# Performance work log

Hardware: AMD Instinct MI355X
Metric: run time of the kernel (lower is better)

## Reference

```python
import jax, jax.numpy as jnp
import numpy as np

B, S, D = 2, 2048, 4096
NH, NKV, HD = 32, 8, 128
N_REP = NH // NKV
MAX_B, MAX_S = 2, 2048


def _rope(x, cos, sin):
    # x: [b, s, h, hd]; cos/sin: [s, hd//2]
    xr = x.reshape(*x.shape[:-1], HD // 2, 2)
    xe, xo = xr[..., 0], xr[..., 1]
    c = cos[None, :, None, :]
    s = sin[None, :, None, :]
    oe = xe * c - xo * s
    oo = xe * s + xo * c
    return jnp.stack([oe, oo], axis=-1).reshape(x.shape)


def setup_inputs() -> dict:
    key = jax.random.key(0)
    ks = jax.random.split(key, 8)
    x = jax.random.normal(ks[0], (B, S, D), dtype=jnp.float32)
    # xavier-normal-ish weights (module uses identity init_method, i.e. uninitialized;
    # we use scaled gaussians for a well-conditioned reference)
    wq = jax.random.normal(ks[1], (NH * HD, D), dtype=jnp.float32) * (1.0 / np.sqrt(D))
    wk = jax.random.normal(ks[2], (NKV * HD, D), dtype=jnp.float32) * (1.0 / np.sqrt(D))
    wv = jax.random.normal(ks[3], (NKV * HD, D), dtype=jnp.float32) * (1.0 / np.sqrt(D))
    wo = jax.random.normal(ks[4], (D, NH * HD), dtype=jnp.float32) * (1.0 / np.sqrt(D))
    # rotary freqs (llama-style, theta=500000)
    theta = 500000.0
    inv = 1.0 / (theta ** (np.arange(0, HD, 2, dtype=np.float32) / HD))  # [hd/2]
    t = np.arange(S, dtype=np.float32)
    ang = np.outer(t, inv)  # [S, hd/2]
    freqs_cos = jnp.asarray(np.cos(ang), dtype=jnp.float32)
    freqs_sin = jnp.asarray(np.sin(ang), dtype=jnp.float32)
    # causal mask
    mask = jnp.where(jnp.tril(jnp.ones((S, S), dtype=bool)), 0.0, -jnp.inf).astype(jnp.float32)
    cache_k = jnp.zeros((MAX_B, MAX_S, NKV, HD), dtype=jnp.float32)
    cache_v = jnp.zeros((MAX_B, MAX_S, NKV, HD), dtype=jnp.float32)
    return {"x": x, "wq": wq, "wk": wk, "wv": wv, "wo": wo,
            "freqs_cos": freqs_cos, "freqs_sin": freqs_sin,
            "mask": mask, "cache_k": cache_k, "cache_v": cache_v,
            "start_pos": 0}


def reference(x, wq, wk, wv, wo, freqs_cos, freqs_sin, mask, cache_k, cache_v, start_pos):
    bsz, seqlen, _ = x.shape
    xq = jnp.einsum('bsd,qd->bsq', x, wq).reshape(bsz, seqlen, NH, HD)
    xk = jnp.einsum('bsd,kd->bsk', x, wk).reshape(bsz, seqlen, NKV, HD)
    xv = jnp.einsum('bsd,vd->bsv', x, wv).reshape(bsz, seqlen, NKV, HD)
    xq = _rope(xq, freqs_cos, freqs_sin)
    xk = _rope(xk, freqs_cos, freqs_sin)
    # KV-cache update then read back valid prefix
    cache_k = jax.lax.dynamic_update_slice(cache_k, xk, (0, start_pos, 0, 0))
    cache_v = jax.lax.dynamic_update_slice(cache_v, xv, (0, start_pos, 0, 0))
    kvlen = start_pos + seqlen
    keys = cache_k[:bsz, :kvlen]    # [b, T, nkv, hd]
    values = cache_v[:bsz, :kvlen]
    # GQA repeat_kv
    keys = jnp.broadcast_to(keys[:, :, :, None, :], (bsz, kvlen, NKV, N_REP, HD)).reshape(bsz, kvlen, NH, HD)
    values = jnp.broadcast_to(values[:, :, :, None, :], (bsz, kvlen, NKV, N_REP, HD)).reshape(bsz, kvlen, NH, HD)
    scores = jnp.einsum('bqhd,bkhd->bhqk', xq, keys) / np.sqrt(HD)
    scores = scores + mask[None, None, :, :]
    probs = jax.nn.softmax(scores, axis=-1)
    out = jnp.einsum('bhqk,bkhd->bqhd', probs, values).reshape(bsz, seqlen, NH * HD)
    return jnp.einsum('bsq,dq->bsd', out, wo)
```

## Files before the change

### kernel.cpp

```cpp
#include <hip/hip_runtime.h>
#include <hip/hip_bf16.h>

#define B_ 2
#define S_ 2048
#define D_ 4096
#define NH_ 32
#define NKV_ 8
#define HD_ 128
#define M_ (B_ * S_)

typedef __bf16 bf16x8_t __attribute__((ext_vector_type(8)));
typedef float f32x4_t __attribute__((ext_vector_type(4)));

__device__ __forceinline__ void gload16(const __bf16* g, __bf16* l) {
  __builtin_amdgcn_global_load_lds(
      (const __attribute__((address_space(1))) void*)g,
      (__attribute__((address_space(3))) void*)l, 16, 0, 0);
}

__global__ __launch_bounds__(256) void convert_main(const float* __restrict__ x,
                                                    const float* __restrict__ wq,
                                                    const float* __restrict__ wk,
                                                    const float* __restrict__ wv,
                                                    __bf16* __restrict__ xb,
                                                    __bf16* __restrict__ wqkv) {
  size_t c = (size_t)blockIdx.x * 256 + threadIdx.x;
  const float* src;
  __bf16* dst;
  if (c < 2097152) { src = x + c * 8; dst = xb + c * 8; }
  else if (c < 4194304) { c -= 2097152; src = wq + c * 8; dst = wqkv + c * 8; }
  else if (c < 4718592) { c -= 4194304; src = wk + c * 8; dst = wqkv + 16777216 + c * 8; }
  else { c -= 4718592; src = wv + c * 8; dst = wqkv + 20971520 + c * 8; }
  const float4* s4 = reinterpret_cast<const float4*>(src);
  float4 a = s4[0], b = s4[1];
  bf16x8_t t;
  t[0] = (__bf16)a.x; t[1] = (__bf16)a.y; t[2] = (__bf16)a.z; t[3] = (__bf16)a.w;
  t[4] = (__bf16)b.x; t[5] = (__bf16)b.y; t[6] = (__bf16)b.z; t[7] = (__bf16)b.w;
  *reinterpret_cast<bf16x8_t*>(dst) = t;
}

__global__ __launch_bounds__(256) void convert_wo(const float* __restrict__ wo,
                                                  __bf16* __restrict__ wob) {
  size_t c = (size_t)blockIdx.x * 256 + threadIdx.x;
  const float4* s4 = reinterpret_cast<const float4*>(wo + c * 8);
  float4 a = s4[0], b = s4[1];
  bf16x8_t t;
  t[0] = (__bf16)a.x; t[1] = (__bf16)a.y; t[2] = (__bf16)a.z; t[3] = (__bf16)a.w;
  t[4] = (__bf16)b.x; t[5] = (__bf16)b.y; t[6] = (__bf16)b.z; t[7] = (__bf16)b.w;
  *reinterpret_cast<bf16x8_t*>(wob + c * 8) = t;
}

template <bool SPLIT, bool OUTF32>
__global__ __launch_bounds__(256) void gemm_bt(const __bf16* __restrict__ A,
                                               const __bf16* __restrict__ Bm,
                                               void* __restrict__ C0,
                                               void* __restrict__ C1,
                                               int N, int K) {
  __shared__ __attribute__((aligned(16))) __bf16 As[128 * 32];
  __shared__ __attribute__((aligned(16))) __bf16 Bs[128 * 32];
  const int tid = threadIdx.x;
  const int lane = tid & 63;
  const int w = tid >> 6;
  const int lo = lane & 15;
  const int hi = lane >> 4;
  const int wm = (w & 1) * 64;
  const int wn = (w >> 1) * 64;
  const int m0 = blockIdx.y * 128;
  const int n0 = blockIdx.x * 128;

  const int srow = w * 32 + (lane >> 2);
  const int scol = (lane & 3) * 8;
  const __bf16* ga0 = A + (size_t)(m0 + srow) * K + scol;
  const __bf16* ga1 = A + (size_t)(m0 + srow + 16) * K + scol;
  const __bf16* gb0 = Bm + (size_t)(n0 + srow) * K + scol;
  const __bf16* gb1 = Bm + (size_t)(n0 + srow + 16) * K + scol;
  __bf16* la0 = &As[(w * 32) * 32];
  __bf16* la1 = &As[(w * 32 + 16) * 32];
  __bf16* lb0 = &Bs[(w * 32) * 32];
  __bf16* lb1 = &Bs[(w * 32 + 16) * 32];

  f32x4_t acc[4][4] = {};

  for (int k0 = 0; k0 < K; k0 += 32) {
    __syncthreads();
    gload16(ga0 + k0, la0);
    gload16(ga1 + k0, la1);
    gload16(gb0 + k0, lb0);
    gload16(gb1 + k0, lb1);
    __syncthreads();
    bf16x8_t af[4], bfr[4];
#pragma unroll
    for (int mi = 0; mi < 4; mi++)
      af[mi] = *reinterpret_cast<const bf16x8_t*>(&As[(wm + mi * 16 + lo) * 32 + hi * 8]);
#pragma unroll
    for (int ni = 0; ni < 4; ni++)
      bfr[ni] = *reinterpret_cast<const bf16x8_t*>(&Bs[(wn + ni * 16 + lo) * 32 + hi * 8]);
#pragma unroll
    for (int mi = 0; mi < 4; mi++)
#pragma unroll
      for (int ni = 0; ni < 4; ni++)
        acc[mi][ni] = __builtin_amdgcn_mfma_f32_16x16x32_bf16(af[mi], bfr[ni], acc[mi][ni], 0, 0, 0);
  }

  __bf16* Cb = nullptr;
  float* Cf = nullptr;
  int ldc, nb;
  if constexpr (SPLIT) {
    if (n0 < 4096) { Cb = (__bf16*)C0; ldc = 4096; nb = n0; }
    else { Cb = (__bf16*)C1; ldc = 2048; nb = n0 - 4096; }
  } else {
    ldc = N; nb = n0;
    if constexpr (OUTF32) Cf = (float*)C0; else Cb = (__bf16*)C0;
  }
#pragma unroll
  for (int mi = 0; mi < 4; mi++) {
    const int mrow = m0 + wm + mi * 16 + hi * 4;
#pragma unroll
    for (int ni = 0; ni < 4; ni++) {
      const int ncol = nb + wn + ni * 16 + lo;
#pragma unroll
      for (int r = 0; r < 4; r++) {
        if constexpr (OUTF32)
          Cf[(size_t)(mrow + r) * ldc + ncol] = acc[mi][ni][r];
        else
          Cb[(size_t)(mrow + r) * ldc + ncol] = (__bf16)acc[mi][ni][r];
      }
    }
  }
}

typedef __bf16 bf16x2_t __attribute__((ext_vector_type(2)));
__global__ __launch_bounds__(256) void rope_kernel(__bf16* __restrict__ q,
                                                   __bf16* __restrict__ kv,
                                                   const float* __restrict__ fcos,
                                                   const float* __restrict__ fsin) {
  const int p = blockIdx.x * 256 + threadIdx.x;
  const int j = p & 63;
  int rem = p >> 6;
  const int hh = rem % (NH_ + NKV_);
  rem /= (NH_ + NKV_);
  const int s = rem % S_;
  const int b = rem / S_;
  const float c = fcos[s * 64 + j];
  const float sn = fsin[s * 64 + j];
  __bf16* base;
  if (hh < NH_)
    base = q + ((size_t)(b * S_ + s) * NH_ + hh) * HD_ + 2 * j;
  else
    base = kv + (size_t)(b * S_ + s) * 2048 + (hh - NH_) * HD_ + 2 * j;
  bf16x2_t xv = *reinterpret_cast<const bf16x2_t*>(base);
  const float xe = (float)xv[0], xo = (float)xv[1];
  bf16x2_t ov;
  ov[0] = (__bf16)(xe * c - xo * sn);
  ov[1] = (__bf16)(xe * sn + xo * c);
  *reinterpret_cast<bf16x2_t*>(base) = ov;
}

__global__ __launch_bounds__(256) void attn_kernel(const __bf16* __restrict__ q,
                                                   const __bf16* __restrict__ kv,
                                                   __bf16* __restrict__ o) {
  const int flat = blockIdx.x + (blockIdx.y << 3) + (blockIdx.z << 8);
  const int hkv = flat & 7;
  const int idx = flat >> 3;
  const int h = hkv * 4 + ((idx >> 3) & 3);
  const int b = idx >> 5;
  const int xpair = idx & 7;

  const int tid = threadIdx.x;
  const int lane = tid & 63;
  const int w = tid >> 6;
  const int lo = lane & 15;
  const int hi = lane >> 4;

  __shared__ __attribute__((aligned(16))) __bf16 Ks[64 * 132];
  __shared__ __attribute__((aligned(16))) __bf16 Vt[128 * 68];
  __shared__ __attribute__((aligned(16))) __bf16 Ps[4][32 * 68];

  bf16x8_t ones;
#pragma unroll
  for (int e = 0; e < 8; e++) ones[e] = (__bf16)1.0f;

  constexpr float SC = 0.08838834764831845f * 1.44269504088896f;

  const __bf16* kvb = kv + (size_t)b * S_ * 2048 + hkv * 128;
  int kkey[4], khc[4], vkey[4], vhc[4];
#pragma unroll
  for (int i = 0; i < 4; i++) {
    const int c = tid + i * 256;
    kkey[i] = c >> 4; khc[i] = c & 15;
    vkey[i] = c & 63; vhc[i] = c >> 6;
  }

  bf16x8_t kreg[4], vreg[4];

  for (int pass = 0; pass < 2; pass++) {
    const int qt = pass ? (15 - xpair) : xpair;
    const int q0 = qt * 128;

    bf16x8_t qf[2][4];
#pragma unroll
    for (int mi = 0; mi < 2; mi++) {
      const size_t qbase = ((size_t)(b * S_ + q0 + w * 32 + mi * 16 + lo) * NH_ + h) * HD_;
#pragma unroll
      for (int ks = 0; ks < 4; ks++)
        qf[mi][ks] = *reinterpret_cast<const bf16x8_t*>(q + qbase + ks * 32 + hi * 8);
    }

    f32x4_t o_acc[2][8] = {};
    f32x4_t l_acc[2] = {};
    float m_prev[2][4];
#pragma unroll
    for (int mi = 0; mi < 2; mi++)
#pragma unroll
      for (int r = 0; r < 4; r++) m_prev[mi][r] = -1e30f;

    const int nkt = qt * 2 + 2;

#pragma unroll
    for (int i = 0; i < 4; i++) {
      kreg[i] = *reinterpret_cast<const bf16x8_t*>(kvb + (size_t)kkey[i] * 2048 + khc[i] * 8);
      vreg[i] = *reinterpret_cast<const bf16x8_t*>(kvb + (size_t)vkey[i] * 2048 + 1024 + vhc[i] * 8);
    }

    for (int kt = 0; kt < nkt; kt++) {
      const int kt0 = kt * 64;
      __syncthreads();
#pragma unroll
      for (int i = 0; i < 4; i++)
        *reinterpret_cast<bf16x8_t*>(&Ks[kkey[i] * 132 + khc[i] * 8]) = kreg[i];
#pragma unroll
      for (int i = 0; i < 4; i++)
#pragma unroll
        for (int e = 0; e < 8; e++) Vt[(vhc[i] * 8 + e) * 68 + vkey[i]] = vreg[i][e];
      __syncthreads();
      if (kt + 1 < nkt) {
        const int nt0 = (kt + 1) * 64;
#pragma unroll
        for (int i = 0; i < 4; i++) {
          kreg[i] = *reinterpret_cast<const bf16x8_t*>(kvb + (size_t)(nt0 + kkey[i]) * 2048 + khc[i] * 8);
          vreg[i] = *reinterpret_cast<const bf16x8_t*>(kvb + (size_t)(nt0 + vkey[i]) * 2048 + 1024 + vhc[i] * 8);
        }
      }

      f32x4_t s_acc[2][4] = {};
      __builtin_amdgcn_s_setprio(1);
#pragma unroll
      for (int ks = 0; ks < 4; ks++) {
        bf16x8_t kf[4];
#pragma unroll
        for (int t = 0; t < 4; t++)
          kf[t] = *reinterpret_cast<const bf16x8_t*>(&Ks[(t * 16 + lo) * 132 + ks * 32 + hi * 8]);
#pragma unroll
        for (int mi = 0; mi < 2; mi++)
#pragma unroll
          for (int t = 0; t < 4; t++)
            s_acc[mi][t] = __builtin_amdgcn_mfma_f32_16x16x32_bf16(qf[mi][ks], kf[t], s_acc[mi][t], 0, 0, 0);
      }
      __builtin_amdgcn_s_setprio(0);

#pragma unroll
      for (int mi = 0; mi < 2; mi++) {
        const int rowbase = q0 + w * 32 + mi * 16;
        const bool need_mask = (kt0 + 63) > rowbase;
        float sv[4][4];
#pragma unroll
        for (int t = 0; t < 4; t++)
#pragma unroll
          for (int r = 0; r < 4; r++) {
            float val = s_acc[mi][t][r] * SC;
            if (need_mask && (kt0 + t * 16 + lo) > (rowbase + hi * 4 + r)) val = -1e30f;
            sv[t][r] = val;
          }
        float alpha[4], mnew[4];
#pragma unroll
        for (int r = 0; r < 4; r++) {
          float mx = fmaxf(fmaxf(sv[0][r], sv[1][r]), fmaxf(sv[2][r], sv[3][r]));
#pragma unroll
          for (int off = 1; off < 16; off <<= 1) mx = fmaxf(mx, __shfl_xor(mx, off));
          mnew[r] = fmaxf(m_prev[mi][r], mx);
          alpha[r] = __builtin_amdgcn_exp2f(m_prev[mi][r] - mnew[r]);
          m_prev[mi][r] = mnew[r];
        }
#pragma unroll
        for (int t = 0; t < 4; t++)
#pragma unroll
          for (int r = 0; r < 4; r++)
            Ps[w][(mi * 16 + hi * 4 + r) * 68 + t * 16 + lo] =
                (__bf16)__builtin_amdgcn_exp2f(sv[t][r] - mnew[r]);
#pragma unroll
        for (int t8 = 0; t8 < 8; t8++)
#pragma unroll
          for (int r = 0; r < 4; r++) o_acc[mi][t8][r] *= alpha[r];
#pragma unroll
        for (int r = 0; r < 4; r++) l_acc[mi][r] *= alpha[r];
      }

      __builtin_amdgcn_s_setprio(1);
#pragma unroll
      for (int ks2 = 0; ks2 < 2; ks2++) {
        bf16x8_t pf[2];
#pragma unroll
        for (int mi = 0; mi < 2; mi++)
          pf[mi] = *reinterpret_cast<const bf16x8_t*>(&Ps[w][(mi * 16 + lo) * 68 + ks2 * 32 + hi * 8]);
#pragma unroll
        for (int mi = 0; mi < 2; mi++)
          l_acc[mi] = __builtin_amdgcn_mfma_f32_16x16x32_bf16(pf[mi], ones, l_acc[mi], 0, 0, 0);
#pragma unroll
        for (int t8 = 0; t8 < 8; t8++) {
          bf16x8_t vf = *reinterpret_cast<const bf16x8_t*>(&Vt[(t8 * 16 + lo) * 68 + ks2 * 32 + hi * 8]);
#pragma unroll
          for (int mi = 0; mi < 2; mi++)
            o_acc[mi][t8] = __builtin_amdgcn_mfma_f32_16x16x32_bf16(pf[mi], vf, o_acc[mi][t8], 0, 0, 0);
        }
      }
      __builtin_amdgcn_s_setprio(0);
    }

#pragma unroll
    for (int mi = 0; mi < 2; mi++)
#pragma unroll
      for (int r = 0; r < 4; r++) {
        const float inv = 1.0f / l_acc[mi][r];
        const int qr = q0 + w * 32 + mi * 16 + hi * 4 + r;
        const size_t obase = ((size_t)(b * S_ + qr) * NH_ + h) * HD_;
#pragma unroll
        for (int t8 = 0; t8 < 8; t8++)
          o[obase + t8 * 16 + lo] = (__bf16)(o_acc[mi][t8][r] * inv);
      }
  }
}

extern "C" void kernel_launch(void* const* d_in, const int* in_sizes, int n_in,
                              void* d_out, int out_size, void* d_ws, size_t ws_size,
                              hipStream_t stream) {
  const float* x = (const float*)d_in[0];
  const float* wq = (const float*)d_in[1];
  const float* wk = (const float*)d_in[2];
  const float* wv = (const float*)d_in[3];
  const float* wo = (const float*)d_in[4];
  const float* fcos = (const float*)d_in[5];
  const float* fsin = (const float*)d_in[6];
  float* out = (float*)d_out;

  __bf16* xb   = (__bf16*)d_ws;
  __bf16* wqkv = xb + (size_t)16777216;
  __bf16* qb   = (__bf16*)d_ws + (size_t)41943040;
  __bf16* kvb  = qb + (size_t)16777216;
  __bf16* wob  = xb;
  __bf16* ab   = wqkv;

  convert_main<<<20480, 256, 0, stream>>>(x, wq, wk, wv, xb, wqkv);
  gemm_bt<true, false><<<dim3(48, 32), 256, 0, stream>>>(xb, wqkv, qb, kvb, 6144, D_);
  convert_wo<<<8192, 256, 0, stream>>>(wo, wob);
  rope_kernel<<<(M_ * (NH_ + NKV_) * (HD_ / 2)) / 256, 256, 0, stream>>>(qb, kvb, fcos, fsin);
  attn_kernel<<<dim3(8, NH_, B_), 256, 0, stream>>>(qb, kvb, ab);
  gemm_bt<false, true><<<dim3(32, 32), 256, 0, stream>>>(ab, wob, out, nullptr, D_, D_);
}
```

Measured before the change: 991.3 us.

## Write V transposed from QKV GEMM and keep P in registers for PV

The QKV GEMM epilogue now writes V directly in a transposed [b, channel, seq] layout and K into its own buffer, so attention can stage V into LDS with vector stores instead of a scalar transpose. Attention computes S^T (K as the A operand), which lets the bf16 probabilities stay in registers as the B operand of 16x16x16 MFMAs, dropping the per-wave P LDS round-trip and the ones-vector MFMA used for row sums. Row max and sum now need only two cross-lane shuffles. The trade-offs are strided 8-byte global writes for V in the GEMM epilogue and twice as many smaller-K MFMAs in the PV product.

```diff
diff --git a/kernel.cpp b/kernel.cpp
--- a/kernel.cpp
+++ b/kernel.cpp
@@ -10,13 +10,29 @@
 #define M_ (B_ * S_)
 
 typedef __bf16 bf16x8_t __attribute__((ext_vector_type(8)));
+typedef __bf16 bf16x4_t __attribute__((ext_vector_type(4)));
+typedef __bf16 bf16x2_t __attribute__((ext_vector_type(2)));
 typedef float f32x4_t __attribute__((ext_vector_type(4)));
+typedef short short4_t __attribute__((ext_vector_type(4)));
 
 __device__ __forceinline__ void gload16(const __bf16* g, __bf16* l) {
   __builtin_amdgcn_global_load_lds(
       (const __attribute__((address_space(1))) void*)g,
       (__attribute__((address_space(3))) void*)l, 16, 0, 0);
 }
+
+#if __has_builtin(__builtin_amdgcn_mfma_f32_16x16x16bf16_1k)
+__device__ __forceinline__ f32x4_t mfma16(bf16x4_t a, bf16x4_t b, f32x4_t c) {
+  return __builtin_amdgcn_mfma_f32_16x16x16bf16_1k(
+      __builtin_bit_cast(short4_t, a), __builtin_bit_cast(short4_t, b), c, 0, 0, 0);
+}
+#else
+__device__ __forceinline__ f32x4_t mfma16(bf16x4_t a, bf16x4_t b, f32x4_t c) {
+  asm("v_mfma_f32_16x16x16_bf16 %0, %1, %2, %0\n\ts_nop 7\n\ts_nop 7"
+      : "+v"(c) : "v"(a), "v"(b));
+  return c;
+}
+#endif
 
 __global__ __launch_bounds__(256) void convert_main(const float* __restrict__ x,
                                                     const float* __restrict__ wq,
@@ -55,6 +71,7 @@
                                                const __bf16* __restrict__ Bm,
                                                void* __restrict__ C0,
                                                void* __restrict__ C1,
+                                               void* __restrict__ C2,
                                                int N, int K) {
   __shared__ __attribute__((aligned(16))) __bf16 As[128 * 32];
   __shared__ __attribute__((aligned(16))) __bf16 Bs[128 * 32];
@@ -102,12 +119,32 @@
         acc[mi][ni] = __builtin_amdgcn_mfma_f32_16x16x32_bf16(af[mi], bfr[ni], acc[mi][ni], 0, 0, 0);
   }
 
+  if constexpr (SPLIT) {
+    if (n0 >= 5120) {
+      __bf16* vtg = (__bf16*)C2;
+#pragma unroll
+      for (int mi = 0; mi < 4; mi++) {
+        const int mrow = m0 + wm + mi * 16 + hi * 4;
+        const int bidx = mrow >> 11;
+        const int s0 = mrow & 2047;
+#pragma unroll
+        for (int ni = 0; ni < 4; ni++) {
+          const int chan = (n0 - 5120) + wn + ni * 16 + lo;
+          bf16x4_t v4;
+#pragma unroll
+          for (int r = 0; r < 4; r++) v4[r] = (__bf16)acc[mi][ni][r];
+          *reinterpret_cast<bf16x4_t*>(vtg + ((size_t)(bidx * 1024 + chan)) * 2048 + s0) = v4;
+        }
+      }
+      return;
+    }
+  }
   __bf16* Cb = nullptr;
   float* Cf = nullptr;
   int ldc, nb;
   if constexpr (SPLIT) {
     if (n0 < 4096) { Cb = (__bf16*)C0; ldc = 4096; nb = n0; }
-    else { Cb = (__bf16*)C1; ldc = 2048; nb = n0 - 4096; }
+    else { Cb = (__bf16*)C1; ldc = 1024; nb = n0 - 4096; }
   } else {
     ldc = N; nb = n0;
     if constexpr (OUTF32) Cf = (float*)C0; else Cb = (__bf16*)C0;
@@ -129,9 +166,8 @@
   }
 }
 
-typedef __bf16 bf16x2_t __attribute__((ext_vector_type(2)));
 __global__ __launch_bounds__(256) void rope_kernel(__bf16* __restrict__ q,
-                                                   __bf16* __restrict__ kv,
+                                                   __bf16* __restrict__ k,
                                                    const float* __restrict__ fcos,
                                                    const float* __restrict__ fsin) {
   const int p = blockIdx.x * 256 + threadIdx.x;
@@ -147,7 +183,7 @@
   if (hh < NH_)
     base = q + ((size_t)(b * S_ + s) * NH_ + hh) * HD_ + 2 * j;
   else
-    base = kv + (size_t)(b * S_ + s) * 2048 + (hh - NH_) * HD_ + 2 * j;
+    base = k + (size_t)(b * S_ + s) * 1024 + (hh - NH_) * HD_ + 2 * j;
   bf16x2_t xv = *reinterpret_cast<const bf16x2_t*>(base);
   const float xe = (float)xv[0], xo = (float)xv[1];
   bf16x2_t ov;
@@ -157,7 +193,8 @@
 }
 
 __global__ __launch_bounds__(256) void attn_kernel(const __bf16* __restrict__ q,
-                                                   const __bf16* __restrict__ kv,
+                                                   const __bf16* __restrict__ k,
+                                                   const __bf16* __restrict__ vt,
                                                    __bf16* __restrict__ o) {
   const int flat = blockIdx.x + (blockIdx.y << 3) + (blockIdx.z << 8);
   const int hkv = flat & 7;
@@ -173,22 +210,18 @@
   const int hi = lane >> 4;
 
   __shared__ __attribute__((aligned(16))) __bf16 Ks[64 * 132];
-  __shared__ __attribute__((aligned(16))) __bf16 Vt[128 * 68];
-  __shared__ __attribute__((aligned(16))) __bf16 Ps[4][32 * 68];
-
-  bf16x8_t ones;
-#pragma unroll
-  for (int e = 0; e < 8; e++) ones[e] = (__bf16)1.0f;
+  __shared__ __attribute__((aligned(16))) __bf16 Vs[128 * 68];
 
   constexpr float SC = 0.08838834764831845f * 1.44269504088896f;
 
-  const __bf16* kvb = kv + (size_t)b * S_ * 2048 + hkv * 128;
-  int kkey[4], khc[4], vkey[4], vhc[4];
+  const __bf16* kbase = k + (size_t)b * S_ * 1024 + hkv * 128;
+  const __bf16* vbase = vt + ((size_t)(b * 1024 + hkv * 128)) * 2048;
+  int kkey[4], khc[4], vhd[4], vkc[4];
 #pragma unroll
   for (int i = 0; i < 4; i++) {
     const int c = tid + i * 256;
     kkey[i] = c >> 4; khc[i] = c & 15;
-    vkey[i] = c & 63; vhc[i] = c >> 6;
+    vhd[i] = c >> 3; vkc[i] = c & 7;
   }
 
   bf16x8_t kreg[4], vreg[4];
@@ -207,42 +240,36 @@
     }
 
     f32x4_t o_acc[2][8] = {};
-    f32x4_t l_acc[2] = {};
-    float m_prev[2][4];
-#pragma unroll
-    for (int mi = 0; mi < 2; mi++)
-#pragma unroll
-      for (int r = 0; r < 4; r++) m_prev[mi][r] = -1e30f;
+    float l_part[2] = {0.f, 0.f};
+    float m_prev[2] = {-1e30f, -1e30f};
 
     const int nkt = qt * 2 + 2;
 
 #pragma unroll
     for (int i = 0; i < 4; i++) {
-      kreg[i] = *reinterpret_cast<const bf16x8_t*>(kvb + (size_t)kkey[i] * 2048 + khc[i] * 8);
-      vreg[i] = *reinterpret_cast<const bf16x8_t*>(kvb + (size_t)vkey[i] * 2048 + 1024 + vhc[i] * 8);
+      kreg[i] = *reinterpret_cast<const bf16x8_t*>(kbase + (size_t)kkey[i] * 1024 + khc[i] * 8);
+      vreg[i] = *reinterpret_cast<const bf16x8_t*>(vbase + (size_t)vhd[i] * 2048 + vkc[i] * 8);
     }
 
     for (int kt = 0; kt < nkt; kt++) {
       const int kt0 = kt * 64;
       __syncthreads();
 #pragma unroll
-      for (int i = 0; i < 4; i++)
+      for (int i = 0; i < 4; i++) {
         *reinterpret_cast<bf16x8_t*>(&Ks[kkey[i] * 132 + khc[i] * 8]) = kreg[i];
-#pragma unroll
-      for (int i = 0; i < 4; i++)
-#pragma unroll
-        for (int e = 0; e < 8; e++) Vt[(vhc[i] * 8 + e) * 68 + vkey[i]] = vreg[i][e];
+        *reinterpret_cast<bf16x8_t*>(&Vs[vhd[i] * 68 + vkc[i] * 8]) = vreg[i];
+      }
       __syncthreads();
       if (kt + 1 < nkt) {
-        const int nt0 = (kt + 1) * 64;
+        const int nt0 = kt0 + 64;
 #pragma unroll
         for (int i = 0; i < 4; i++) {
-          kreg[i] = *reinterpret_cast<const bf16x8_t*>(kvb + (size_t)(nt0 + kkey[i]) * 2048 + khc[i] * 8);
-          vreg[i] = *reinterpret_cast<const bf16x8_t*>(kvb + (size_t)(nt0 + vkey[i]) * 2048 + 1024 + vhc[i] * 8);
+          kreg[i] = *reinterpret_cast<const bf16x8_t*>(kbase + (size_t)(nt0 + kkey[i]) * 1024 + khc[i] * 8);
+          vreg[i] = *reinterpret_cast<const bf16x8_t*>(vbase + (size_t)vhd[i] * 2048 + nt0 + vkc[i] * 8);
         }
       }
 
-      f32x4_t s_acc[2][4] = {};
+      f32x4_t s2[4][2] = {};
       __builtin_amdgcn_s_setprio(1);
 #pragma unroll
       for (int ks = 0; ks < 4; ks++) {
@@ -251,82 +278,81 @@
         for (int t = 0; t < 4; t++)
           kf[t] = *reinterpret_cast<const bf16x8_t*>(&Ks[(t * 16 + lo) * 132 + ks * 32 + hi * 8]);
 #pragma unroll
-        for (int mi = 0; mi < 2; mi++)
-#pragma unroll
-          for (int t = 0; t < 4; t++)
-            s_acc[mi][t] = __builtin_amdgcn_mfma_f32_16x16x32_bf16(qf[mi][ks], kf[t], s_acc[mi][t], 0, 0, 0);
+        for (int t = 0; t < 4; t++)
+#pragma unroll
+          for (int mi = 0; mi < 2; mi++)
+            s2[t][mi] = __builtin_amdgcn_mfma_f32_16x16x32_bf16(kf[t], qf[mi][ks], s2[t][mi], 0, 0, 0);
       }
       __builtin_amdgcn_s_setprio(0);
 
+      bf16x4_t pb[2][4];
 #pragma unroll
       for (int mi = 0; mi < 2; mi++) {
-        const int rowbase = q0 + w * 32 + mi * 16;
-        const bool need_mask = (kt0 + 63) > rowbase;
+        const int qrow = q0 + w * 32 + mi * 16 + lo;
+        const bool need_mask = (kt0 + 63) > (q0 + w * 32 + mi * 16);
         float sv[4][4];
 #pragma unroll
         for (int t = 0; t < 4; t++)
 #pragma unroll
           for (int r = 0; r < 4; r++) {
-            float val = s_acc[mi][t][r] * SC;
-            if (need_mask && (kt0 + t * 16 + lo) > (rowbase + hi * 4 + r)) val = -1e30f;
+            float val = s2[t][mi][r] * SC;
+            if (need_mask && (kt0 + t * 16 + hi * 4 + r) > qrow) val = -1e30f;
             sv[t][r] = val;
           }
-        float alpha[4], mnew[4];
-#pragma unroll
-        for (int r = 0; r < 4; r++) {
-          float mx = fmaxf(fmaxf(sv[0][r], sv[1][r]), fmaxf(sv[2][r], sv[3][r]));
-#pragma unroll
-          for (int off = 1; off < 16; off <<= 1) mx = fmaxf(mx, __shfl_xor(mx, off));
-          mnew[r] = fmaxf(m_prev[mi][r], mx);
-          alpha[r] = __builtin_amdgcn_exp2f(m_prev[mi][r] - mnew[r]);
-          m_prev[mi][r] = mnew[r];
+        float mx = sv[0][0];
+#pragma unroll
+        for (int t = 0; t < 4; t++)
+#pragma unroll
+          for (int r = 0; r < 4; r++) mx = fmaxf(mx, sv[t][r]);
+        mx = fmaxf(mx, __shfl_xor(mx, 16));
+        mx = fmaxf(mx, __shfl_xor(mx, 32));
+        const float mnew = fmaxf(m_prev[mi], mx);
+        const float alpha = __builtin_amdgcn_exp2f(m_prev[mi] - mnew);
+        m_prev[mi] = mnew;
+        float psum = 0.f;
+#pragma unroll
+        for (int t = 0; t < 4; t++)
+#pragma unroll
+          for (int r = 0; r < 4; r++) {
+            const float p = __builtin_amdgcn_exp2f(sv[t][r] - mnew);
+            psum += p;
+            pb[mi][t][r] = (__bf16)p;
+          }
+        l_part[mi] = l_part[mi] * alpha + psum;
+#pragma unroll
+        for (int t8 = 0; t8 < 8; t8++) o_acc[mi][t8] *= alpha;
+      }
+
+      __builtin_amdgcn_s_setprio(1);
+#pragma unroll
+      for (int t = 0; t < 4; t++) {
+#pragma unroll
+        for (int t8 = 0; t8 < 8; t8++) {
+          bf16x4_t va = *reinterpret_cast<const bf16x4_t*>(&Vs[(t8 * 16 + lo) * 68 + t * 16 + hi * 4]);
+#pragma unroll
+          for (int mi = 0; mi < 2; mi++)
+            o_acc[mi][t8] = mfma16(va, pb[mi][t], o_acc[mi][t8]);
         }
-#pragma unroll
-        for (int t = 0; t < 4; t++)
-#pragma unroll
-          for (int r = 0; r < 4; r++)
-            Ps[w][(mi * 16 + hi * 4 + r) * 68 + t * 16 + lo] =
-                (__bf16)__builtin_amdgcn_exp2f(sv[t][r] - mnew[r]);
-#pragma unroll
-        for (int t8 = 0; t8 < 8; t8++)
-#pragma unroll
-          for (int r = 0; r < 4; r++) o_acc[mi][t8][r] *= alpha[r];
-#pragma unroll
-        for (int r = 0; r < 4; r++) l_acc[mi][r] *= alpha[r];
-      }
-
-      __builtin_amdgcn_s_setprio(1);
-#pragma unroll
-      for (int ks2 = 0; ks2 < 2; ks2++) {
-        bf16x8_t pf[2];
-#pragma unroll
-        for (int mi = 0; mi < 2; mi++)
-          pf[mi] = *reinterpret_cast<const bf16x8_t*>(&Ps[w][(mi * 16 + lo) * 68 + ks2 * 32 + hi * 8]);
-#pragma unroll
-        for (int mi = 0; mi < 2; mi++)
-          l_acc[mi] = __builtin_amdgcn_mfma_f32_16x16x32_bf16(pf[mi], ones, l_acc[mi], 0, 0, 0);
-#pragma unroll
-        for (int t8 = 0; t8 < 8; t8++) {
-          bf16x8_t vf = *reinterpret_cast<const bf16x8_t*>(&Vt[(t8 * 16 + lo) * 68 + ks2 * 32 + hi * 8]);
-#pragma unroll
-          for (int mi = 0; mi < 2; mi++)
-            o_acc[mi][t8] = __builtin_amdgcn_mfma_f32_16x16x32_bf16(pf[mi], vf, o_acc[mi][t8], 0, 0, 0);
-        }
       }
       __builtin_amdgcn_s_setprio(0);
     }
 
 #pragma unroll
-    for (int mi = 0; mi < 2; mi++)
-#pragma unroll
-      for (int r = 0; r < 4; r++) {
-        const float inv = 1.0f / l_acc[mi][r];
-        const int qr = q0 + w * 32 + mi * 16 + hi * 4 + r;
-        const size_t obase = ((size_t)(b * S_ + qr) * NH_ + h) * HD_;
-#pragma unroll
-        for (int t8 = 0; t8 < 8; t8++)
-          o[obase + t8 * 16 + lo] = (__bf16)(o_acc[mi][t8][r] * inv);
-      }
+    for (int mi = 0; mi < 2; mi++) {
+      float l = l_part[mi];
+      l += __shfl_xor(l, 16);
+      l += __shfl_xor(l, 32);
+      const float inv = 1.0f / l;
+      const int qr = q0 + w * 32 + mi * 16 + lo;
+      const size_t obase = ((size_t)(b * S_ + qr) * NH_ + h) * HD_ + hi * 4;
+#pragma unroll
+      for (int t8 = 0; t8 < 8; t8++) {
+        bf16x4_t ov;
+#pragma unroll
+        for (int r = 0; r < 4; r++) ov[r] = (__bf16)(o_acc[mi][t8][r] * inv);
+        *reinterpret_cast<bf16x4_t*>(o + obase + t8 * 16) = ov;
+      }
+    }
   }
 }
 
@@ -346,13 +372,14 @@
   __bf16* wqkv = xb + (size_t)16777216;
   __bf16* qb   = (__bf16*)d_ws + (size_t)41943040;
   __bf16* kvb  = qb + (size_t)16777216;
+  __bf16* vtg  = kvb + (size_t)4194304;
   __bf16* wob  = xb;
   __bf16* ab   = wqkv;
 
   convert_main<<<20480, 256, 0, stream>>>(x, wq, wk, wv, xb, wqkv);
-  gemm_bt<true, false><<<dim3(48, 32), 256, 0, stream>>>(xb, wqkv, qb, kvb, 6144, D_);
+  gemm_bt<true, false><<<dim3(48, 32), 256, 0, stream>>>(xb, wqkv, qb, kvb, vtg, 6144, D_);
   convert_wo<<<8192, 256, 0, stream>>>(wo, wob);
   rope_kernel<<<(M_ * (NH_ + NKV_) * (HD_ / 2)) / 256, 256, 0, stream>>>(qb, kvb, fcos, fsin);
-  attn_kernel<<<dim3(8, NH_, B_), 256, 0, stream>>>(qb, kvb, ab);
-  gemm_bt<false, true><<<dim3(32, 32), 256, 0, stream>>>(ab, wob, out, nullptr, D_, D_);
-}
+  attn_kernel<<<dim3(8, NH_, B_), 256, 0, stream>>>(qb, kvb, vtg, ab);
+  gemm_bt<false, true><<<dim3(32, 32), 256, 0, stream>>>(ab, wob, out, nullptr, nullptr, D_, D_);
+}
```

Result: faster. 894.5 us (-9.8%).
